# Optimization experiments

Hardware: AMD Instinct MI355X
Metric: run time of the kernel (lower is better)

The kernel has to match this reference:

```python
import jax, jax.numpy as jnp
import numpy as np

BLOCK_SIZE = 32       # MXFP block size (OCP microscaling spec)
E2M1_MAX = 6.0        # max magnitude representable in FP4 E2M1
E2M1_EMAX = 2.0       # exponent of max binade (4..6)


def quantize_mxfp4(t):
    """Fake-quantize t to MXFP4 (E2M1 elements, E8M0 shared scale) along last dim.

    Matches MXFP_F.extract_mxfp_components + dequant: per block of 32 values a
    power-of-two shared scale 2^(floor(log2(amax)) - emax_elem), elements
    rounded to nearest E2M1 value {0, +-0.5, 1, 1.5, 2, 3, 4, 6}.
    """
    shp = t.shape
    tb = t.reshape(shp[:-1] + (shp[-1] // BLOCK_SIZE, BLOCK_SIZE))
    amax = jnp.max(jnp.abs(tb), axis=-1, keepdims=True)
    safe_amax = jnp.where(amax > 0, amax, 1.0)
    shared_exp = jnp.floor(jnp.log2(safe_amax)) - E2M1_EMAX  # E8M0 exponent
    scale = jnp.exp2(shared_exp)
    v = tb / scale
    av = jnp.abs(v)
    # E2M1 grid spacing: 0.5 in [0,2), 1 in [2,4), 2 in [4,6]
    e = jnp.clip(jnp.floor(jnp.log2(jnp.maximum(av, 2.0 ** -10))), 0.0, E2M1_EMAX)
    step = jnp.exp2(e - 1.0)  # one mantissa bit
    q = jnp.clip(jnp.round(av / step) * step, 0.0, E2M1_MAX) * jnp.sign(v)
    return (q * scale).reshape(shp)


def setup_inputs() -> dict:
    key = jax.random.key(0)
    kx, kw, kb = jax.random.split(key, 3)
    B, S, K, N = 2, 4096, 4096, 4096
    x = jax.random.normal(kx, (B, S, K), dtype=jnp.float32)
    weight = jax.random.normal(kw, (N, K), dtype=jnp.float32) * 0.02
    bias = jax.random.normal(kb, (N,), dtype=jnp.float32) * 0.02
    return {"x": x, "weight": weight, "bias": bias}


def reference(x, weight, bias):
    # layer_type 'XqWqB': quantize activations (block along in_features) and
    # weights (block_dim=1 == in_features); bias stays full precision.
    xq = quantize_mxfp4(x)                 # [B, S, K]
    wq = quantize_mxfp4(weight)            # [N, K]
    out = jnp.einsum("bsk,nk->bsn", xq, wq) + bias
    return out
```

## Files before the change

### kernel.cpp

```cpp
#include <hip/hip_runtime.h>
#include <hip/hip_bf16.h>

typedef __attribute__((ext_vector_type(4))) int i32x4;
typedef __attribute__((ext_vector_type(8))) int i32x8;
typedef __attribute__((ext_vector_type(16))) float f32x16;

#define GLOBAL_CPTR(x) ((__attribute__((address_space(1))) const void*)(x))
#define LDS_PTR(x)     ((__attribute__((address_space(3))) void*)(x))

__global__ __launch_bounds__(256) void mxfp4_quant_pack_kernel(
    const float* __restrict__ in, unsigned char* __restrict__ outq,
    unsigned char* __restrict__ outsc, int kshift, long long n) {
  long long e = ((long long)blockIdx.x * 256 + threadIdx.x) * 8;
  if (e >= n) return;

  float4 v0 = *reinterpret_cast<const float4*>(in + e);
  float4 v1 = *reinterpret_cast<const float4*>(in + e + 4);
  float vv[8] = {v0.x, v0.y, v0.z, v0.w, v1.x, v1.y, v1.z, v1.w};
  float am = 0.f;
#pragma unroll
  for (int j = 0; j < 8; ++j) am = fmaxf(am, fabsf(vv[j]));
  am = fmaxf(am, __shfl_xor(am, 1, 64));
  am = fmaxf(am, __shfl_xor(am, 2, 64));

  float safe = am > 0.f ? am : 1.f;
  int se = ilogbf(safe) - 2;
  float inv = ldexpf(1.f, -se);

  unsigned int pack = 0;
#pragma unroll
  for (int j = 0; j < 8; ++j) {
    float val = vv[j] * inv;
    float av = fabsf(val);
    float avc = fmaxf(av, 9.765625e-4f);
    int ee = (int)((__float_as_uint(avc) >> 23) & 0xFF) - 127;
    ee = ee < 0 ? 0 : (ee > 2 ? 2 : ee);
    float step  = ldexpf(1.f, ee - 1);
    float istep = ldexpf(1.f, 1 - ee);
    float q = rintf(av * istep) * step;
    q = fminf(q, 6.f);
    unsigned int c = q >= 5.f   ? 7u
                   : q >= 3.5f  ? 6u
                   : q >= 2.5f  ? 5u
                   : q >= 1.75f ? 4u
                   : q >= 1.25f ? 3u
                   : q >= 0.75f ? 2u
                   : q >= 0.25f ? 1u : 0u;
    if (val < 0.f) c |= 8u;
    pack |= c << (4 * j);
  }

  const int row = (int)(e >> kshift);
  const int k = (int)(e & ((1 << kshift) - 1));
  const size_t chunk = (size_t)(row >> 8) * (size_t)(1 << (kshift - 5)) + (k >> 5);
  *(unsigned int*)(outq + chunk * 4096 + (size_t)(row & 255) * 16 +
                   ((k & 31) >> 1)) = pack;
  if ((threadIdx.x & 3) == 0) {
    outsc[chunk * 256 + (row & 31) * 8 + ((row >> 5) & 7)] =
        (unsigned char)(se + 127);
  }
}

#define BM 256
#define BN 256
#define NTHR 512
#define BUFS 34816

__global__ __launch_bounds__(NTHR, 2) void mxfp_gemm_kernel(
    const unsigned char* __restrict__ Aq, const unsigned char* __restrict__ Asc,
    const unsigned char* __restrict__ Bq, const unsigned char* __restrict__ Bsc,
    const float* __restrict__ bias, float* __restrict__ C,
    int M, int N, int K) {
  __shared__ unsigned char lds[2 * BUFS];

  const int tid = threadIdx.x;
  const int l   = tid & 63;
  const int wid = tid >> 6;
  const int wm  = wid >> 2;
  const int wn  = wid & 3;

  const int nwg = gridDim.x;
  const int bid = blockIdx.x;
  const int swz = (bid & 7) * (nwg >> 3) + (bid >> 3);
  const int nbn = N / BN;
  const int bm  = swz / nbn;
  const int bn  = swz % nbn;

  const int KC = K >> 5;

  f32x16 acc[4][2] = {};

#define STAGE(BUFO, KT)                                                        \
  do {                                                                         \
    const int cl = wid & 3;                                                    \
    const int rg2 = (wid >> 2) << 1;                                           \
    const size_t abase = ((size_t)bm * KC + (size_t)(KT) * 4 + cl) * 4096;     \
    const size_t bbase = ((size_t)bn * KC + (size_t)(KT) * 4 + cl) * 4096;     \
    _Pragma("unroll") for (int i = 0; i < 2; ++i) {                            \
      __builtin_amdgcn_global_load_lds(                                        \
          GLOBAL_CPTR(Aq + abase + (rg2 + i) * 1024 + (l << 4)),               \
          LDS_PTR(lds + (BUFO) + cl * 4096 + (rg2 + i) * 1024), 16, 0, 0);     \
      __builtin_amdgcn_global_load_lds(                                        \
          GLOBAL_CPTR(Bq + bbase + (rg2 + i) * 1024 + (l << 4)),               \
          LDS_PTR(lds + (BUFO) + 16384 + cl * 4096 + (rg2 + i) * 1024),        \
          16, 0, 0);                                                           \
    }                                                                          \
    if (wid < 4) {                                                             \
      __builtin_amdgcn_global_load_lds(                                        \
          GLOBAL_CPTR(Asc + ((size_t)bm * KC + (size_t)(KT) * 4 + wid) * 256   \
                      + (l << 2)),                                             \
          LDS_PTR(lds + (BUFO) + 32768 + wid * 256), 4, 0, 0);                 \
    } else {                                                                   \
      __builtin_amdgcn_global_load_lds(                                        \
          GLOBAL_CPTR(Bsc + ((size_t)bn * KC + (size_t)(KT) * 4 + (wid - 4))   \
                      * 256 + (l << 2)),                                       \
          LDS_PTR(lds + (BUFO) + 33792 + (wid - 4) * 256), 4, 0, 0);           \
    }                                                                          \
  } while (0)

#define KTILE(BUFO)                                                            \
  do {                                                                         \
    const i32x4 z4 = {0, 0, 0, 0};                                             \
    _Pragma("unroll") for (int ks = 0; ks < 2; ++ks) {                         \
      const int cofs = (ks << 13) + ((l & 32) << 7);    \
      i32x8 a8[4], b8[2];                                                      \
      int sa[4], sb[2];                                                        \
      _Pragma("unroll") for (int mb = 0; mb < 4; ++mb)                         \
        a8[mb] = __builtin_shufflevector(                                      \
            *(const i32x4*)(lds + (BUFO) + cofs +                              \
                            (((wm << 7) + (mb << 5) + (l & 31)) << 4)),        \
            z4, 0, 1, 2, 3, 4, 5, 6, 7);                                       \
      _Pragma("unroll") for (int nb = 0; nb < 2; ++nb)                         \
        b8[nb] = __builtin_shufflevector(                                      \
            *(const i32x4*)(lds + (BUFO) + 16384 + cofs +                      \
                            (((wn << 6) + (nb << 5) + (l & 31)) << 4)),        \
            z4, 0, 1, 2, 3, 4, 5, 6, 7);                                       \
      const int av = *(const int*)(lds + (BUFO) + 32768 + (cofs >> 4) +        \
                                   ((l & 31) << 3) + (wm << 2));               \
      const int bv = *(const ushort*)(lds + (BUFO) + 33792 + (cofs >> 4) +     \
                                      ((l & 31) << 3) + (wn << 1));            \
      _Pragma("unroll") for (int mb = 0; mb < 4; ++mb)                         \
        sa[mb] = (int)((unsigned)((av >> (mb << 3)) & 255) * 0x01010101u);     \
      _Pragma("unroll") for (int nb = 0; nb < 2; ++nb)                         \
        sb[nb] = (int)((unsigned)((bv >> (nb << 3)) & 255) * 0x01010101u);     \
      _Pragma("unroll") for (int mb = 0; mb < 4; ++mb)                         \
        _Pragma("unroll") for (int nb = 0; nb < 2; ++nb)                       \
          acc[mb][nb] = __builtin_amdgcn_mfma_scale_f32_32x32x64_f8f6f4(       \
              a8[mb], b8[nb], acc[mb][nb], 4, 4, 0, sa[mb], 0, sb[nb]);        \
    }                                                                          \
  } while (0)

  STAGE(0, 0);
  asm volatile("s_waitcnt vmcnt(0)" ::: "memory");
  __builtin_amdgcn_s_barrier();
  asm volatile("" ::: "memory");

  const int NKT = K >> 7;
  for (int t = 0; t < NKT; ++t) {
    const int tn = (t + 1 < NKT) ? (t + 1) : t;
    const int bufC = (t & 1) ? BUFS : 0;
    const int bufN = (t & 1) ? 0 : BUFS;
    STAGE(bufN, tn);
    KTILE(bufC);
    asm volatile("s_waitcnt vmcnt(0)" ::: "memory");
    __builtin_amdgcn_s_barrier();
    asm volatile("" ::: "memory");
  }

  const int colb = bn * BN + wn * 64 + (l & 31);
  const int rowb = bm * BM + wm * 128 + ((l >> 5) << 2);
  const float bv0 = bias[colb];
  const float bv1 = bias[colb + 32];
#pragma unroll
  for (int mb = 0; mb < 4; ++mb) {
#pragma unroll
    for (int nb = 0; nb < 2; ++nb) {
      const float bv = nb ? bv1 : bv0;
      const int col = colb + nb * 32;
#pragma unroll
      for (int r = 0; r < 16; ++r) {
        const int row = rowb + mb * 32 + ((r >> 2) << 3) + (r & 3);
        C[(size_t)row * N + col] = acc[mb][nb][r] + bv;
      }
    }
  }
}

extern "C" void kernel_launch(void* const* d_in, const int* in_sizes, int n_in,
                              void* d_out, int out_size, void* d_ws, size_t ws_size,
                              hipStream_t stream) {
  const float* x    = (const float*)d_in[0];
  const float* w    = (const float*)d_in[1];
  const float* bias = (const float*)d_in[2];
  float* out = (float*)d_out;

  const int N = in_sizes[2];
  const int K = in_sizes[1] / N;
  const int M = (int)((long long)in_sizes[0] / K);
  const int kshift = __builtin_ctz(K);

  unsigned char* xq  = (unsigned char*)d_ws;
  unsigned char* wq  = xq + ((size_t)M * K >> 1);
  unsigned char* xsc = wq + ((size_t)N * K >> 1);
  unsigned char* wsc = xsc + ((size_t)M * K >> 5);

  const long long nx = (long long)M * K;
  const long long nw = (long long)N * K;

  mxfp4_quant_pack_kernel<<<dim3((unsigned)(nx / 2048)), dim3(256), 0, stream>>>(
      x, xq, xsc, kshift, nx);
  mxfp4_quant_pack_kernel<<<dim3((unsigned)(nw / 2048)), dim3(256), 0, stream>>>(
      w, wq, wsc, kshift, nw);

  dim3 grid((M / BM) * (N / BN));
  mxfp_gemm_kernel<<<grid, dim3(NTHR), 0, stream>>>(xq, xsc, wq, wsc, bias, out,
                                                    M, N, K);
}
```

Baseline: 151.7 us.

## Halve GEMM M-tile for higher occupancy and rewrite quantizer as per-thread blocks

The GEMM tile shrinks from 256x256 to 128x256. The LDS buffer is cut and launch bounds are raised to 4 workgroups per CU, so more tiles run per CU and the grid is larger, giving better wave coverage on the GPU. The quantizer now has each thread handle a full 32-element block. That removes the cross-lane shuffles and writes 16-byte packed outputs, but each thread's global reads now use a large row stride. The smaller M tile halves reuse of B per tile and raises global traffic for the weights.

```diff
diff --git a/kernel.cpp b/kernel.cpp
--- a/kernel.cpp
+++ b/kernel.cpp
@@ -10,27 +10,33 @@
 
 __global__ __launch_bounds__(256) void mxfp4_quant_pack_kernel(
     const float* __restrict__ in, unsigned char* __restrict__ outq,
-    unsigned char* __restrict__ outsc, int kshift, long long n) {
-  long long e = ((long long)blockIdx.x * 256 + threadIdx.x) * 8;
-  if (e >= n) return;
-
-  float4 v0 = *reinterpret_cast<const float4*>(in + e);
-  float4 v1 = *reinterpret_cast<const float4*>(in + e + 4);
-  float vv[8] = {v0.x, v0.y, v0.z, v0.w, v1.x, v1.y, v1.z, v1.w};
+    unsigned char* __restrict__ outsc, int kshift) {
+  const int KC = 1 << (kshift - 5);
+  const int bid = blockIdx.x;
+  const int kc = bid & (KC - 1);
+  const int rp = bid >> (kshift - 5);
+  const int r  = threadIdx.x;
+  const long long row = ((long long)rp << 8) + r;
+  const float* src = in + (row << kshift) + (kc << 5);
+
+  float v[32];
+#pragma unroll
+  for (int i = 0; i < 8; ++i)
+    *reinterpret_cast<float4*>(v + 4 * i) =
+        *reinterpret_cast<const float4*>(src + 4 * i);
+
   float am = 0.f;
 #pragma unroll
-  for (int j = 0; j < 8; ++j) am = fmaxf(am, fabsf(vv[j]));
-  am = fmaxf(am, __shfl_xor(am, 1, 64));
-  am = fmaxf(am, __shfl_xor(am, 2, 64));
+  for (int j = 0; j < 32; ++j) am = fmaxf(am, fabsf(v[j]));
 
   float safe = am > 0.f ? am : 1.f;
   int se = ilogbf(safe) - 2;
   float inv = ldexpf(1.f, -se);
 
-  unsigned int pack = 0;
-#pragma unroll
-  for (int j = 0; j < 8; ++j) {
-    float val = vv[j] * inv;
+  unsigned int packs[4] = {0, 0, 0, 0};
+#pragma unroll
+  for (int j = 0; j < 32; ++j) {
+    float val = v[j] * inv;
     float av = fabsf(val);
     float avc = fmaxf(av, 9.765625e-4f);
     int ee = (int)((__float_as_uint(avc) >> 23) & 0xFF) - 127;
@@ -47,26 +53,21 @@
                    : q >= 0.75f ? 2u
                    : q >= 0.25f ? 1u : 0u;
     if (val < 0.f) c |= 8u;
-    pack |= c << (4 * j);
+    packs[j >> 3] |= c << (4 * (j & 7));
   }
 
-  const int row = (int)(e >> kshift);
-  const int k = (int)(e & ((1 << kshift) - 1));
-  const size_t chunk = (size_t)(row >> 8) * (size_t)(1 << (kshift - 5)) + (k >> 5);
-  *(unsigned int*)(outq + chunk * 4096 + (size_t)(row & 255) * 16 +
-                   ((k & 31) >> 1)) = pack;
-  if ((threadIdx.x & 3) == 0) {
-    outsc[chunk * 256 + (row & 31) * 8 + ((row >> 5) & 7)] =
-        (unsigned char)(se + 127);
-  }
+  const size_t chunk = (size_t)rp * KC + kc;
+  *reinterpret_cast<uint4*>(outq + chunk * 4096 + (size_t)r * 16) =
+      make_uint4(packs[0], packs[1], packs[2], packs[3]);
+  outsc[chunk * 256 + (r & 31) * 8 + (r >> 5)] = (unsigned char)(se + 127);
 }
 
-#define BM 256
+#define BM 128
 #define BN 256
 #define NTHR 512
-#define BUFS 34816
-
-__global__ __launch_bounds__(NTHR, 2) void mxfp_gemm_kernel(
+#define BUFS 26624
+
+__global__ __launch_bounds__(NTHR, 4) void mxfp_gemm_kernel(
     const unsigned char* __restrict__ Aq, const unsigned char* __restrict__ Asc,
     const unsigned char* __restrict__ Bq, const unsigned char* __restrict__ Bsc,
     const float* __restrict__ bias, float* __restrict__ C,
@@ -88,33 +89,37 @@
 
   const int KC = K >> 5;
 
-  f32x16 acc[4][2] = {};
+  f32x16 acc[2][2] = {};
 
 #define STAGE(BUFO, KT)                                                        \
   do {                                                                         \
-    const int cl = wid & 3;                                                    \
-    const int rg2 = (wid >> 2) << 1;                                           \
-    const size_t abase = ((size_t)bm * KC + (size_t)(KT) * 4 + cl) * 4096;     \
-    const size_t bbase = ((size_t)bn * KC + (size_t)(KT) * 4 + cl) * 4096;     \
-    _Pragma("unroll") for (int i = 0; i < 2; ++i) {                            \
+    const size_t kcb = (size_t)(KT) * 4;                                       \
+    _Pragma("unroll") for (int jj = 0; jj < 2; ++jj) {                         \
+      const int jb = wid * 2 + jj;                                             \
+      const int cb = jb >> 2, qb = jb & 3;                                     \
       __builtin_amdgcn_global_load_lds(                                        \
-          GLOBAL_CPTR(Aq + abase + (rg2 + i) * 1024 + (l << 4)),               \
-          LDS_PTR(lds + (BUFO) + cl * 4096 + (rg2 + i) * 1024), 16, 0, 0);     \
-      __builtin_amdgcn_global_load_lds(                                        \
-          GLOBAL_CPTR(Bq + bbase + (rg2 + i) * 1024 + (l << 4)),               \
-          LDS_PTR(lds + (BUFO) + 16384 + cl * 4096 + (rg2 + i) * 1024),        \
-          16, 0, 0);                                                           \
+          GLOBAL_CPTR(Bq + (((size_t)bn * KC + kcb + cb) << 12) +              \
+                      (qb << 10) + (l << 4)),                                  \
+          LDS_PTR(lds + (BUFO) + 8192 + cb * 4096 + qb * 1024), 16, 0, 0);     \
     }                                                                          \
     if (wid < 4) {                                                             \
+      _Pragma("unroll") for (int jj = 0; jj < 2; ++jj) {                       \
+        const int ja = wid * 2 + jj;                                           \
+        const int ca = ja >> 1, ha = ja & 1;                                   \
+        __builtin_amdgcn_global_load_lds(                                      \
+            GLOBAL_CPTR(Aq + (((size_t)(bm >> 1) * KC + kcb + ca) << 12) +     \
+                        ((bm & 1) << 11) + (ha << 10) + (l << 4)),             \
+            LDS_PTR(lds + (BUFO) + ca * 2048 + ha * 1024), 16, 0, 0);          \
+      }                                                                        \
+    } else {                                                                   \
+      const int cs = wid - 4;                                                  \
       __builtin_amdgcn_global_load_lds(                                        \
-          GLOBAL_CPTR(Asc + ((size_t)bm * KC + (size_t)(KT) * 4 + wid) * 256   \
-                      + (l << 2)),                                             \
-          LDS_PTR(lds + (BUFO) + 32768 + wid * 256), 4, 0, 0);                 \
-    } else {                                                                   \
+          GLOBAL_CPTR(Asc + (((size_t)(bm >> 1) * KC + kcb + cs) << 8) +       \
+                      (l << 2)),                                               \
+          LDS_PTR(lds + (BUFO) + 24576 + cs * 256), 4, 0, 0);                  \
       __builtin_amdgcn_global_load_lds(                                        \
-          GLOBAL_CPTR(Bsc + ((size_t)bn * KC + (size_t)(KT) * 4 + (wid - 4))   \
-                      * 256 + (l << 2)),                                       \
-          LDS_PTR(lds + (BUFO) + 33792 + (wid - 4) * 256), 4, 0, 0);           \
+          GLOBAL_CPTR(Bsc + (((size_t)bn * KC + kcb + cs) << 8) + (l << 2)),   \
+          LDS_PTR(lds + (BUFO) + 25600 + cs * 256), 4, 0, 0);                  \
     }                                                                          \
   } while (0)
 
@@ -122,28 +127,30 @@
   do {                                                                         \
     const i32x4 z4 = {0, 0, 0, 0};                                             \
     _Pragma("unroll") for (int ks = 0; ks < 2; ++ks) {                         \
-      const int cofs = (ks << 13) + ((l & 32) << 7);    \
-      i32x8 a8[4], b8[2];                                                      \
-      int sa[4], sb[2];                                                        \
-      _Pragma("unroll") for (int mb = 0; mb < 4; ++mb)                         \
+      const int cc = (ks << 1) + (l >> 5);       \
+      i32x8 a8[2], b8[2];                                                      \
+      int sa[2], sb[2];                                                        \
+      _Pragma("unroll") for (int mb = 0; mb < 2; ++mb)                         \
         a8[mb] = __builtin_shufflevector(                                      \
-            *(const i32x4*)(lds + (BUFO) + cofs +                              \
-                            (((wm << 7) + (mb << 5) + (l & 31)) << 4)),        \
+            *(const i32x4*)(lds + (BUFO) + cc * 2048 +                         \
+                            ((wm * 64 + mb * 32 + (l & 31)) << 4)),            \
             z4, 0, 1, 2, 3, 4, 5, 6, 7);                                       \
       _Pragma("unroll") for (int nb = 0; nb < 2; ++nb)                         \
         b8[nb] = __builtin_shufflevector(                                      \
-            *(const i32x4*)(lds + (BUFO) + 16384 + cofs +                      \
-                            (((wn << 6) + (nb << 5) + (l & 31)) << 4)),        \
+            *(const i32x4*)(lds + (BUFO) + 8192 + cc * 4096 +                  \
+                            ((wn * 64 + nb * 32 + (l & 31)) << 4)),            \
             z4, 0, 1, 2, 3, 4, 5, 6, 7);                                       \
-      const int av = *(const int*)(lds + (BUFO) + 32768 + (cofs >> 4) +        \
-                                   ((l & 31) << 3) + (wm << 2));               \
-      const int bv = *(const ushort*)(lds + (BUFO) + 33792 + (cofs >> 4) +     \
-                                      ((l & 31) << 3) + (wn << 1));            \
-      _Pragma("unroll") for (int mb = 0; mb < 4; ++mb)                         \
-        sa[mb] = (int)((unsigned)((av >> (mb << 3)) & 255) * 0x01010101u);     \
+      const int av = *(const int*)(lds + (BUFO) + 24576 + cc * 256 +           \
+                                   ((l & 31) << 3) + ((bm & 1) << 2));         \
+      const int bv = *(const int*)(lds + (BUFO) + 25600 + cc * 256 +           \
+                                   ((l & 31) << 3) + ((wn >> 1) << 2));        \
+      _Pragma("unroll") for (int mb = 0; mb < 2; ++mb)                         \
+        sa[mb] = (int)((unsigned)((av >> (((wm << 1) + mb) << 3)) & 255) *     \
+                       0x01010101u);                                           \
       _Pragma("unroll") for (int nb = 0; nb < 2; ++nb)                         \
-        sb[nb] = (int)((unsigned)((bv >> (nb << 3)) & 255) * 0x01010101u);     \
-      _Pragma("unroll") for (int mb = 0; mb < 4; ++mb)                         \
+        sb[nb] = (int)((unsigned)((bv >> ((((wn & 1) << 1) + nb) << 3)) & 255) \
+                       * 0x01010101u);                                         \
+      _Pragma("unroll") for (int mb = 0; mb < 2; ++mb)                         \
         _Pragma("unroll") for (int nb = 0; nb < 2; ++nb)                       \
           acc[mb][nb] = __builtin_amdgcn_mfma_scale_f32_32x32x64_f8f6f4(       \
               a8[mb], b8[nb], acc[mb][nb], 4, 4, 0, sa[mb], 0, sb[nb]);        \
@@ -168,15 +175,13 @@
   }
 
   const int colb = bn * BN + wn * 64 + (l & 31);
-  const int rowb = bm * BM + wm * 128 + ((l >> 5) << 2);
-  const float bv0 = bias[colb];
-  const float bv1 = bias[colb + 32];
-#pragma unroll
-  for (int mb = 0; mb < 4; ++mb) {
+  const int rowb = bm * BM + wm * 64 + ((l >> 5) << 2);
+#pragma unroll
+  for (int mb = 0; mb < 2; ++mb) {
 #pragma unroll
     for (int nb = 0; nb < 2; ++nb) {
-      const float bv = nb ? bv1 : bv0;
       const int col = colb + nb * 32;
+      const float bv = bias[col];
 #pragma unroll
       for (int r = 0; r < 16; ++r) {
         const int row = rowb + mb * 32 + ((r >> 2) << 3) + (r & 3);
@@ -207,10 +212,10 @@
   const long long nx = (long long)M * K;
   const long long nw = (long long)N * K;
 
-  mxfp4_quant_pack_kernel<<<dim3((unsigned)(nx / 2048)), dim3(256), 0, stream>>>(
-      x, xq, xsc, kshift, nx);
-  mxfp4_quant_pack_kernel<<<dim3((unsigned)(nw / 2048)), dim3(256), 0, stream>>>(
-      w, wq, wsc, kshift, nw);
+  mxfp4_quant_pack_kernel<<<dim3((unsigned)(nx / 8192)), dim3(256), 0, stream>>>(
+      x, xq, xsc, kshift);
+  mxfp4_quant_pack_kernel<<<dim3((unsigned)(nw / 8192)), dim3(256), 0, stream>>>(
+      w, wq, wsc, kshift);
 
   dim3 grid((M / BM) * (N / BN));
   mxfp_gemm_kernel<<<grid, dim3(NTHR), 0, stream>>>(xq, xsc, wq, wsc, bias, out,
```

Result: slower. 171.3 us (+12.9%).

## Restage MXFP4 quantization through LDS so each thread owns a full block

Applied to the files above, without the earlier changes.

The quantize-pack kernel now loads a 64x128 float tile into shared memory with coalesced float4 reads. Each thread then processes one whole 32-element block, which removes the cross-lane shuffles and lets it write a 16-byte packed store plus one scale byte. The E2M1 encoding is also simplified to integer arithmetic instead of a comparison chain. This is meant to cut scattered 4-byte stores and ALU work in the memory-bound quant pass, at the cost of LDS traffic and a sync. The new launch grid assumes M and N are multiples of 64 and K is a multiple of 128.

```diff
diff --git a/kernel.cpp b/kernel.cpp
--- a/kernel.cpp
+++ b/kernel.cpp
@@ -10,55 +10,67 @@
 
 __global__ __launch_bounds__(256) void mxfp4_quant_pack_kernel(
     const float* __restrict__ in, unsigned char* __restrict__ outq,
-    unsigned char* __restrict__ outsc, int kshift, long long n) {
-  long long e = ((long long)blockIdx.x * 256 + threadIdx.x) * 8;
-  if (e >= n) return;
-
-  float4 v0 = *reinterpret_cast<const float4*>(in + e);
-  float4 v1 = *reinterpret_cast<const float4*>(in + e + 4);
-  float vv[8] = {v0.x, v0.y, v0.z, v0.w, v1.x, v1.y, v1.z, v1.w};
+    unsigned char* __restrict__ outsc, int kshift) {
+  const int KC = 1 << (kshift - 5);
+  const int CQ = KC >> 2;
+  const int bid = blockIdx.x;
+  const int cq  = bid & (CQ - 1);
+  const int R   = (bid >> (kshift - 7)) << 6;
+  const int t   = threadIdx.x;
+
+  __shared__ float sf[64 * 132];
+
+  const float* base = in + ((size_t)R << kshift) + (cq << 7);
+#pragma unroll
+  for (int i = 0; i < 8; ++i) {
+    const int g   = i * 256 + t;
+    const int row = g >> 5;
+    const int c4  = g & 31;
+    float4 v = *reinterpret_cast<const float4*>(
+        base + ((size_t)row << kshift) + (c4 << 2));
+    *reinterpret_cast<float4*>(sf + row * 132 + (c4 << 2)) = v;
+  }
+  __syncthreads();
+
+  const int rl = (t & 3) + ((t >> 4) << 2);
+  const int kc = (t >> 2) & 3;
+  const float* src = sf + rl * 132 + (kc << 5);
+  float v[32];
+#pragma unroll
+  for (int i = 0; i < 8; ++i)
+    *reinterpret_cast<float4*>(v + 4 * i) =
+        *reinterpret_cast<const float4*>(src + 4 * i);
+
   float am = 0.f;
 #pragma unroll
-  for (int j = 0; j < 8; ++j) am = fmaxf(am, fabsf(vv[j]));
-  am = fmaxf(am, __shfl_xor(am, 1, 64));
-  am = fmaxf(am, __shfl_xor(am, 2, 64));
-
-  float safe = am > 0.f ? am : 1.f;
-  int se = ilogbf(safe) - 2;
-  float inv = ldexpf(1.f, -se);
-
-  unsigned int pack = 0;
-#pragma unroll
-  for (int j = 0; j < 8; ++j) {
-    float val = vv[j] * inv;
-    float av = fabsf(val);
-    float avc = fmaxf(av, 9.765625e-4f);
+  for (int j = 0; j < 32; ++j) am = fmaxf(am, fabsf(v[j]));
+
+  const float safe = am > 0.f ? am : 1.f;
+  const int se = ilogbf(safe) - 2;
+  const float inv = ldexpf(1.f, -se);
+
+  unsigned int packs[4] = {0, 0, 0, 0};
+#pragma unroll
+  for (int j = 0; j < 32; ++j) {
+    const float val = v[j] * inv;
+    const float av = fabsf(val);
+    const float avc = fmaxf(av, 9.765625e-4f);
     int ee = (int)((__float_as_uint(avc) >> 23) & 0xFF) - 127;
     ee = ee < 0 ? 0 : (ee > 2 ? 2 : ee);
-    float step  = ldexpf(1.f, ee - 1);
-    float istep = ldexpf(1.f, 1 - ee);
-    float q = rintf(av * istep) * step;
-    q = fminf(q, 6.f);
-    unsigned int c = q >= 5.f   ? 7u
-                   : q >= 3.5f  ? 6u
-                   : q >= 2.5f  ? 5u
-                   : q >= 1.75f ? 4u
-                   : q >= 1.25f ? 3u
-                   : q >= 0.75f ? 2u
-                   : q >= 0.25f ? 1u : 0u;
-    if (val < 0.f) c |= 8u;
-    pack |= c << (4 * j);
-  }
-
-  const int row = (int)(e >> kshift);
-  const int k = (int)(e & ((1 << kshift) - 1));
-  const size_t chunk = (size_t)(row >> 8) * (size_t)(1 << (kshift - 5)) + (k >> 5);
-  *(unsigned int*)(outq + chunk * 4096 + (size_t)(row & 255) * 16 +
-                   ((k & 31) >> 1)) = pack;
-  if ((threadIdx.x & 3) == 0) {
-    outsc[chunk * 256 + (row & 31) * 8 + ((row >> 5) & 7)] =
-        (unsigned char)(se + 127);
-  }
+    const float istep = __uint_as_float((unsigned)(128 - ee) << 23);
+    const int m = (int)rintf(av * istep);
+    unsigned int c = (unsigned)(m + (ee << 1));
+    c = c > 7u ? 7u : c;
+    c |= (__float_as_uint(val) >> 28) & 8u;
+    packs[j >> 3] |= c << (4 * (j & 7));
+  }
+
+  const int row = R + rl;
+  const size_t chunk = (size_t)(row >> 8) * KC + (cq << 2) + kc;
+  *reinterpret_cast<uint4*>(outq + chunk * 4096 + (size_t)(row & 255) * 16) =
+      make_uint4(packs[0], packs[1], packs[2], packs[3]);
+  outsc[chunk * 256 + (row & 31) * 8 + ((row >> 5) & 7)] =
+      (unsigned char)(se + 127);
 }
 
 #define BM 256
@@ -204,13 +216,12 @@
   unsigned char* xsc = wq + ((size_t)N * K >> 1);
   unsigned char* wsc = xsc + ((size_t)M * K >> 5);
 
-  const long long nx = (long long)M * K;
-  const long long nw = (long long)N * K;
-
-  mxfp4_quant_pack_kernel<<<dim3((unsigned)(nx / 2048)), dim3(256), 0, stream>>>(
-      x, xq, xsc, kshift, nx);
-  mxfp4_quant_pack_kernel<<<dim3((unsigned)(nw / 2048)), dim3(256), 0, stream>>>(
-      w, wq, wsc, kshift, nw);
+  const int CQ = (K >> 5) >> 2;
+
+  mxfp4_quant_pack_kernel<<<dim3((unsigned)((M >> 6) * CQ)), dim3(256), 0,
+                            stream>>>(x, xq, xsc, kshift);
+  mxfp4_quant_pack_kernel<<<dim3((unsigned)((N >> 6) * CQ)), dim3(256), 0,
+                            stream>>>(w, wq, wsc, kshift);
 
   dim3 grid((M / BM) * (N / BN));
   mxfp_gemm_kernel<<<grid, dim3(NTHR), 0, stream>>>(xq, xsc, wq, wsc, bias, out,
```

Result: faster. 140.2 us (-7.6%).
